# Kernel optimization log

Hardware: AMD Instinct MI355X
Metric: run time of the kernel (lower is better)

## Reference

```python
import jax, jax.numpy as jnp
import numpy as np

N_NODES = 50000
N_EDGES = 600000
F_IN = 128
F_HID = 128
F_OUT = 2


def setup_inputs() -> dict:
    key = jax.random.key(0)
    k_x, k_e, k_w1, k_w2 = jax.random.split(key, 4)
    x = jax.random.normal(k_x, (N_NODES, F_IN), dtype=jnp.float32)
    edge_index = jax.random.randint(k_e, (2, N_EDGES), 0, N_NODES, dtype=jnp.int32)
    # Glorot-style init for the GCNConv linear weights
    W1 = jax.random.normal(k_w1, (F_IN, F_HID), dtype=jnp.float32) * (1.0 / np.sqrt(F_IN))
    b1 = jnp.zeros((F_HID,), dtype=jnp.float32)
    W2 = jax.random.normal(k_w2, (F_HID, F_OUT), dtype=jnp.float32) * (1.0 / np.sqrt(F_HID))
    b2 = jnp.zeros((F_OUT,), dtype=jnp.float32)
    return {"x": x, "edge_index": edge_index, "W1": W1, "b1": b1, "W2": W2, "b2": b2}


def reference(x, edge_index, W1, b1, W2, b2):
    n = x.shape[0]
    # Add self-loops: A_tilde = A + I
    loops = jnp.arange(n, dtype=edge_index.dtype)
    src = jnp.concatenate([edge_index[0], loops])
    dst = jnp.concatenate([edge_index[1], loops])
    # Symmetric normalization: D^{-1/2} A_tilde D^{-1/2}
    deg = jax.ops.segment_sum(jnp.ones_like(dst, dtype=x.dtype), dst, num_segments=n)
    dinv = jnp.where(deg > 0, jax.lax.rsqrt(deg), 0.0)
    w = dinv[src] * dinv[dst]  # [E+N] per-edge norm coefficient

    def gcn_conv(h, W, b):
        h = h @ W  # transform first (small GEMM), then aggregate
        msg = h[src] * w[:, None]  # gather + scale, [E+N, F]
        return jax.ops.segment_sum(msg, dst, num_segments=n) + b

    h = jax.nn.relu(gcn_conv(x, W1, b1))
    # dropout is identity in eval mode
    return gcn_conv(h, W2, b2)
```

## Files before the change

kernel.cpp:

```cpp
#include <hip/hip_runtime.h>

#define N_NODES 50000
#define N_EDGES 600000
#define F 128
#define BCAP 64

typedef __attribute__((ext_vector_type(8))) short bf16x8;
typedef __attribute__((ext_vector_type(4))) float f32x4;

__device__ inline unsigned short bf16rn(float f) {
  unsigned u = __float_as_uint(f);
  return (unsigned short)((u + 0x7FFFu + ((u >> 16) & 1u)) >> 16);
}
__device__ inline float bflo(unsigned u) { return __uint_as_float(u << 16); }
__device__ inline float bfhi(unsigned u) { return __uint_as_float(u & 0xFFFF0000u); }

__global__ __launch_bounds__(256) void k_init(int* __restrict__ cnt, const float* __restrict__ W,
                                              ushort* __restrict__ wt, ushort* __restrict__ h,
                                              float* __restrict__ h2) {
  int i = blockIdx.x * 256 + threadIdx.x;
  if (i < N_NODES) cnt[i] = 0;
  if (i < F * F) {
    int n = i >> 7;
    int k = i & 127;
    wt[n * 128 + k] = bf16rn(W[k * 128 + n]);
  }
  if (i < F) h[(size_t)N_NODES * F + i] = 0;
  if (i == 0) { h2[2 * N_NODES] = 0.f; h2[2 * N_NODES + 1] = 0.f; }
}

__global__ __launch_bounds__(256) void k_fill(const int* __restrict__ ei, int* __restrict__ cnt,
                                              ushort* __restrict__ csr) {
  int e0 = (blockIdx.x * 256 + threadIdx.x) * 4;
  if (e0 >= N_EDGES) return;
  int4 s = *(const int4*)&ei[e0];
  int4 d = *(const int4*)&ei[N_EDGES + e0];
  int p0 = atomicAdd(&cnt[d.x], 1);
  int p1 = atomicAdd(&cnt[d.y], 1);
  int p2 = atomicAdd(&cnt[d.z], 1);
  int p3 = atomicAdd(&cnt[d.w], 1);
  if (p0 < BCAP) csr[d.x * BCAP + p0] = (ushort)s.x;
  if (p1 < BCAP) csr[d.y * BCAP + p1] = (ushort)s.y;
  if (p2 < BCAP) csr[d.z * BCAP + p2] = (ushort)s.z;
  if (p3 < BCAP) csr[d.w * BCAP + p3] = (ushort)s.w;
}

__global__ __launch_bounds__(256) void k_nodeinit(const int* __restrict__ cnt, float* __restrict__ dinv,
                                                  ushort* __restrict__ csr) {
  int i = blockIdx.x * 256 + threadIdx.x;
  if (i >= N_NODES) return;
  int c = min(cnt[i], BCAP);
  dinv[i] = rsqrtf((float)(c + 1));
  int npad = (c + 7) & ~7;
  for (int j = c; j < npad; ++j) csr[i * BCAP + j] = (ushort)N_NODES;
}

__global__ __launch_bounds__(256) void k_gemm1(const float* __restrict__ x, const ushort* __restrict__ wt_g,
                                               const float* __restrict__ dinv, ushort* __restrict__ h) {
  __shared__ ushort xs[64 * 128];
  __shared__ ushort wt[128 * 128];
  int t = threadIdx.x;
  int row0 = blockIdx.x * 64;

  {
    int r = t >> 2, q = t & 3;
    bool ok = (row0 + r) < N_NODES;
    const float4* xg = (const float4*)(x + (size_t)(row0 + r) * F + q * 32);
    unsigned pk[16];
    #pragma unroll
    for (int j = 0; j < 8; ++j) {
      float4 v = ok ? xg[j] : make_float4(0.f, 0.f, 0.f, 0.f);
      pk[2 * j]     = (unsigned)bf16rn(v.x) | ((unsigned)bf16rn(v.y) << 16);
      pk[2 * j + 1] = (unsigned)bf16rn(v.z) | ((unsigned)bf16rn(v.w) << 16);
    }
    #pragma unroll
    for (int j2 = 0; j2 < 4; ++j2) {
      int off = r * 256 + (((q * 64 + j2 * 16) ^ ((r & 7) << 4)));
      *(uint4*)((char*)xs + off) = make_uint4(pk[4 * j2], pk[4 * j2 + 1], pk[4 * j2 + 2], pk[4 * j2 + 3]);
    }
  }
  {
    int n = t >> 1, hf = t & 1;
    const uint4* wg = (const uint4*)(wt_g + n * 128);
    #pragma unroll
    for (int j = 0; j < 8; ++j) {
      uint4 v = wg[hf * 8 + j];
      int off = n * 256 + (((hf * 128 + j * 16) ^ ((n & 7) << 4)));
      *(uint4*)((char*)wt + off) = v;
    }
  }
  __syncthreads();

  int w = t >> 6;
  int lane = t & 63;
  int m = lane & 15;
  int kb = lane >> 4;
  int rloc = w * 16 + m;

  bf16x8 af[4];
  #pragma unroll
  for (int ks = 0; ks < 4; ++ks) {
    int off = rloc * 256 + (((ks * 64 + kb * 16) ^ ((rloc & 7) << 4)));
    af[ks] = *(bf16x8*)((char*)xs + off);
  }

  f32x4 acc[8];
  #pragma unroll
  for (int nf = 0; nf < 8; ++nf) acc[nf] = (f32x4){0.f, 0.f, 0.f, 0.f};

  #pragma unroll
  for (int nf = 0; nf < 8; ++nf) {
    int ncol = nf * 16 + m;
    #pragma unroll
    for (int ks = 0; ks < 4; ++ks) {
      int off = ncol * 256 + (((ks * 64 + kb * 16) ^ ((ncol & 7) << 4)));
      bf16x8 bfr = *(bf16x8*)((char*)wt + off);
      acc[nf] = __builtin_amdgcn_mfma_f32_16x16x32_bf16(af[ks], bfr, acc[nf], 0, 0, 0);
    }
  }

  int rbase = row0 + w * 16 + kb * 4;
  float di[4];
  #pragma unroll
  for (int reg = 0; reg < 4; ++reg) di[reg] = (rbase + reg < N_NODES) ? dinv[rbase + reg] : 0.f;
  #pragma unroll
  for (int nf = 0; nf < 8; ++nf) {
    #pragma unroll
    for (int reg = 0; reg < 4; ++reg) {
      int rr = rbase + reg;
      if (rr < N_NODES) h[(size_t)rr * F + nf * 16 + m] = bf16rn(di[reg] * acc[nf][reg]);
    }
  }
}

__global__ __launch_bounds__(256) void k_agg1(const uint4* __restrict__ h, const int* __restrict__ cnt,
                                              const float* __restrict__ dinv,
                                              const ushort* __restrict__ csr,
                                              const float* __restrict__ b1, const float* __restrict__ W2,
                                              float* __restrict__ h2) {
  int tid = threadIdx.x;
  int lane16 = tid & 15;
  int node = blockIdx.x * 16 + (tid >> 4);
  float di = dinv[node];
  uint4 su = h[(size_t)node * 16 + lane16];
  float a0 = bflo(su.x), a1 = bfhi(su.x), a2 = bflo(su.y), a3 = bfhi(su.y);
  float a4 = bflo(su.z), a5 = bfhi(su.z), a6 = bflo(su.w), a7 = bfhi(su.w);
  int base = node * BCAP;
  int npad = (min(cnt[node], BCAP) + 7) & ~7;
  for (int e = 0; e < npad; e += 8) {
    int s0 = csr[base + e + 0];
    int s1 = csr[base + e + 1];
    int s2 = csr[base + e + 2];
    int s3 = csr[base + e + 3];
    int s4 = csr[base + e + 4];
    int s5 = csr[base + e + 5];
    int s6 = csr[base + e + 6];
    int s7 = csr[base + e + 7];
    uint4 u0 = h[(size_t)s0 * 16 + lane16];
    uint4 u1 = h[(size_t)s1 * 16 + lane16];
    uint4 u2 = h[(size_t)s2 * 16 + lane16];
    uint4 u3 = h[(size_t)s3 * 16 + lane16];
    uint4 u4 = h[(size_t)s4 * 16 + lane16];
    uint4 u5 = h[(size_t)s5 * 16 + lane16];
    uint4 u6 = h[(size_t)s6 * 16 + lane16];
    uint4 u7 = h[(size_t)s7 * 16 + lane16];
    a0 += bflo(u0.x); a1 += bfhi(u0.x); a2 += bflo(u0.y); a3 += bfhi(u0.y);
    a4 += bflo(u0.z); a5 += bfhi(u0.z); a6 += bflo(u0.w); a7 += bfhi(u0.w);
    a0 += bflo(u1.x); a1 += bfhi(u1.x); a2 += bflo(u1.y); a3 += bfhi(u1.y);
    a4 += bflo(u1.z); a5 += bfhi(u1.z); a6 += bflo(u1.w); a7 += bfhi(u1.w);
    a0 += bflo(u2.x); a1 += bfhi(u2.x); a2 += bflo(u2.y); a3 += bfhi(u2.y);
    a4 += bflo(u2.z); a5 += bfhi(u2.z); a6 += bflo(u2.w); a7 += bfhi(u2.w);
    a0 += bflo(u3.x); a1 += bfhi(u3.x); a2 += bflo(u3.y); a3 += bfhi(u3.y);
    a4 += bflo(u3.z); a5 += bfhi(u3.z); a6 += bflo(u3.w); a7 += bfhi(u3.w);
    a0 += bflo(u4.x); a1 += bfhi(u4.x); a2 += bflo(u4.y); a3 += bfhi(u4.y);
    a4 += bflo(u4.z); a5 += bfhi(u4.z); a6 += bflo(u4.w); a7 += bfhi(u4.w);
    a0 += bflo(u5.x); a1 += bfhi(u5.x); a2 += bflo(u5.y); a3 += bfhi(u5.y);
    a4 += bflo(u5.z); a5 += bfhi(u5.z); a6 += bflo(u5.w); a7 += bfhi(u5.w);
    a0 += bflo(u6.x); a1 += bfhi(u6.x); a2 += bflo(u6.y); a3 += bfhi(u6.y);
    a4 += bflo(u6.z); a5 += bfhi(u6.z); a6 += bflo(u6.w); a7 += bfhi(u6.w);
    a0 += bflo(u7.x); a1 += bfhi(u7.x); a2 += bflo(u7.y); a3 += bfhi(u7.y);
    a4 += bflo(u7.z); a5 += bfhi(u7.z); a6 += bflo(u7.w); a7 += bfhi(u7.w);
  }
  float4 bb0 = ((const float4*)b1)[2 * lane16];
  float4 bb1 = ((const float4*)b1)[2 * lane16 + 1];
  float o0 = fmaxf(fmaf(di, a0, bb0.x), 0.f);
  float o1 = fmaxf(fmaf(di, a1, bb0.y), 0.f);
  float o2 = fmaxf(fmaf(di, a2, bb0.z), 0.f);
  float o3 = fmaxf(fmaf(di, a3, bb0.w), 0.f);
  float o4 = fmaxf(fmaf(di, a4, bb1.x), 0.f);
  float o5 = fmaxf(fmaf(di, a5, bb1.y), 0.f);
  float o6 = fmaxf(fmaf(di, a6, bb1.z), 0.f);
  float o7 = fmaxf(fmaf(di, a7, bb1.w), 0.f);

  const float2* W2v = (const float2*)W2;
  float2 w0 = W2v[8 * lane16 + 0], w1 = W2v[8 * lane16 + 1];
  float2 w2 = W2v[8 * lane16 + 2], w3 = W2v[8 * lane16 + 3];
  float2 w4 = W2v[8 * lane16 + 4], w5 = W2v[8 * lane16 + 5];
  float2 w6 = W2v[8 * lane16 + 6], w7 = W2v[8 * lane16 + 7];
  float c0 = fmaf(o0, w0.x, fmaf(o1, w1.x, fmaf(o2, w2.x, fmaf(o3, w3.x,
             fmaf(o4, w4.x, fmaf(o5, w5.x, fmaf(o6, w6.x, o7 * w7.x)))))));
  float c1 = fmaf(o0, w0.y, fmaf(o1, w1.y, fmaf(o2, w2.y, fmaf(o3, w3.y,
             fmaf(o4, w4.y, fmaf(o5, w5.y, fmaf(o6, w6.y, o7 * w7.y)))))));
  #pragma unroll
  for (int mask = 1; mask < 16; mask <<= 1) {
    c0 += __shfl_xor(c0, mask, 64);
    c1 += __shfl_xor(c1, mask, 64);
  }
  if (lane16 == 0) ((float2*)h2)[node] = make_float2(di * c0, di * c1);
}

__global__ __launch_bounds__(256) void k_agg2(const float* __restrict__ h2, const int* __restrict__ cnt,
                                              const float* __restrict__ dinv,
                                              const ushort* __restrict__ csr,
                                              const float* __restrict__ b2, float* __restrict__ out) {
  int i = blockIdx.x * 256 + threadIdx.x;
  if (i >= N_NODES) return;
  float di = dinv[i];
  const float2* hp = (const float2*)h2;
  float2 self = hp[i];
  float ax = self.x;
  float ay = self.y;
  int base = i * BCAP;
  int npad = (min(cnt[i], BCAP) + 3) & ~3;
  for (int e = 0; e < npad; e += 4) {
    int a = csr[base + e + 0];
    int b = csr[base + e + 1];
    int c = csr[base + e + 2];
    int d = csr[base + e + 3];
    float2 v0 = hp[a];
    float2 v1 = hp[b];
    float2 v2 = hp[c];
    float2 v3 = hp[d];
    ax += v0.x; ay += v0.y;
    ax += v1.x; ay += v1.y;
    ax += v2.x; ay += v2.y;
    ax += v3.x; ay += v3.y;
  }
  ((float2*)out)[i] = make_float2(fmaf(di, ax, b2[0]), fmaf(di, ay, b2[1]));
}

extern "C" void kernel_launch(void* const* d_in, const int* in_sizes, int n_in,
                              void* d_out, int out_size, void* d_ws, size_t ws_size,
                              hipStream_t stream) {
  const float* x  = (const float*)d_in[0];
  const int*   ei = (const int*)d_in[1];
  const float* W1 = (const float*)d_in[2];
  const float* b1 = (const float*)d_in[3];
  const float* W2 = (const float*)d_in[4];
  const float* b2 = (const float*)d_in[5];
  float* out = (float*)d_out;

  char* w = (char*)d_ws;
  auto alloc = [&](size_t bytes) {
    char* p = w;
    w += (bytes + 255) & ~size_t(255);
    return p;
  };
  int*    cnt  = (int*)alloc(N_NODES * 4);
  float*  dinv = (float*)alloc(N_NODES * 4);
  ushort* csr  = (ushort*)alloc((size_t)N_NODES * BCAP * 2);
  ushort* wt   = (ushort*)alloc((size_t)F * F * 2);
  ushort* h    = (ushort*)alloc((size_t)(N_NODES + 1) * F * 2);
  float*  h2   = (float*)alloc((size_t)(N_NODES + 1) * 2 * 4);

  k_init<<<196, 256, 0, stream>>>(cnt, W1, wt, h, h2);
  k_fill<<<586, 256, 0, stream>>>(ei, cnt, csr);
  k_nodeinit<<<196, 256, 0, stream>>>(cnt, dinv, csr);
  k_gemm1<<<782, 256, 0, stream>>>(x, wt, dinv, h);
  k_agg1<<<3125, 256, 0, stream>>>((const uint4*)h, cnt, dinv, csr, b1, W2, h2);
  k_agg2<<<196, 256, 0, stream>>>(h2, cnt, dinv, csr, b2, out);
}
```

Before: 95.30 us.

## Fuse node-init into GEMM1 and vectorize CSR index loads in aggregations

Folds the degree-normalization and CSR padding step into the GEMM kernel prologue, which removes one kernel launch and lets the per-row dinv come from shared memory. The aggregation kernels now read 8 (or 4) 16-bit neighbor indices with a single vector load instead of separate scalar loads. k_fill handles 8 edges per thread with half as many blocks. The gemm1 prologue adds a serial padding loop on 64 threads, and its dinv reads depend on an existing barrier in the GEMM body.

```diff
diff --git a/kernel.cpp b/kernel.cpp
--- a/kernel.cpp
+++ b/kernel.cpp
@@ -31,36 +31,50 @@
 
 __global__ __launch_bounds__(256) void k_fill(const int* __restrict__ ei, int* __restrict__ cnt,
                                               ushort* __restrict__ csr) {
-  int e0 = (blockIdx.x * 256 + threadIdx.x) * 4;
+  int e0 = (blockIdx.x * 256 + threadIdx.x) * 8;
   if (e0 >= N_EDGES) return;
-  int4 s = *(const int4*)&ei[e0];
-  int4 d = *(const int4*)&ei[N_EDGES + e0];
-  int p0 = atomicAdd(&cnt[d.x], 1);
-  int p1 = atomicAdd(&cnt[d.y], 1);
-  int p2 = atomicAdd(&cnt[d.z], 1);
-  int p3 = atomicAdd(&cnt[d.w], 1);
-  if (p0 < BCAP) csr[d.x * BCAP + p0] = (ushort)s.x;
-  if (p1 < BCAP) csr[d.y * BCAP + p1] = (ushort)s.y;
-  if (p2 < BCAP) csr[d.z * BCAP + p2] = (ushort)s.z;
-  if (p3 < BCAP) csr[d.w * BCAP + p3] = (ushort)s.w;
-}
-
-__global__ __launch_bounds__(256) void k_nodeinit(const int* __restrict__ cnt, float* __restrict__ dinv,
-                                                  ushort* __restrict__ csr) {
-  int i = blockIdx.x * 256 + threadIdx.x;
-  if (i >= N_NODES) return;
-  int c = min(cnt[i], BCAP);
-  dinv[i] = rsqrtf((float)(c + 1));
-  int npad = (c + 7) & ~7;
-  for (int j = c; j < npad; ++j) csr[i * BCAP + j] = (ushort)N_NODES;
+  int4 sa = *(const int4*)&ei[e0];
+  int4 sb = *(const int4*)&ei[e0 + 4];
+  int4 da = *(const int4*)&ei[N_EDGES + e0];
+  int4 db = *(const int4*)&ei[N_EDGES + e0 + 4];
+  int p0 = atomicAdd(&cnt[da.x], 1);
+  int p1 = atomicAdd(&cnt[da.y], 1);
+  int p2 = atomicAdd(&cnt[da.z], 1);
+  int p3 = atomicAdd(&cnt[da.w], 1);
+  int p4 = atomicAdd(&cnt[db.x], 1);
+  int p5 = atomicAdd(&cnt[db.y], 1);
+  int p6 = atomicAdd(&cnt[db.z], 1);
+  int p7 = atomicAdd(&cnt[db.w], 1);
+  if (p0 < BCAP) csr[da.x * BCAP + p0] = (ushort)sa.x;
+  if (p1 < BCAP) csr[da.y * BCAP + p1] = (ushort)sa.y;
+  if (p2 < BCAP) csr[da.z * BCAP + p2] = (ushort)sa.z;
+  if (p3 < BCAP) csr[da.w * BCAP + p3] = (ushort)sa.w;
+  if (p4 < BCAP) csr[db.x * BCAP + p4] = (ushort)sb.x;
+  if (p5 < BCAP) csr[db.y * BCAP + p5] = (ushort)sb.y;
+  if (p6 < BCAP) csr[db.z * BCAP + p6] = (ushort)sb.z;
+  if (p7 < BCAP) csr[db.w * BCAP + p7] = (ushort)sb.w;
 }
 
 __global__ __launch_bounds__(256) void k_gemm1(const float* __restrict__ x, const ushort* __restrict__ wt_g,
-                                               const float* __restrict__ dinv, ushort* __restrict__ h) {
+                                               const int* __restrict__ cnt, float* __restrict__ dinv,
+                                               ushort* __restrict__ csr, ushort* __restrict__ h) {
   __shared__ ushort xs[64 * 128];
   __shared__ ushort wt[128 * 128];
+  __shared__ float dinv_lds[64];
   int t = threadIdx.x;
   int row0 = blockIdx.x * 64;
+
+  if (t < 64) {
+    int node = row0 + t;
+    if (node < N_NODES) {
+      int c = min(cnt[node], BCAP);
+      float d = rsqrtf((float)(c + 1));
+      dinv_lds[t] = d;
+      dinv[node] = d;
+      int npad = (c + 7) & ~7;
+      for (int j = c; j < npad; ++j) csr[node * BCAP + j] = (ushort)N_NODES;
+    }
+  }
 
   {
     int r = t >> 2, q = t & 3;
@@ -120,15 +134,15 @@
   }
 
   int rbase = row0 + w * 16 + kb * 4;
-  float di[4];
-  #pragma unroll
-  for (int reg = 0; reg < 4; ++reg) di[reg] = (rbase + reg < N_NODES) ? dinv[rbase + reg] : 0.f;
   #pragma unroll
   for (int nf = 0; nf < 8; ++nf) {
     #pragma unroll
     for (int reg = 0; reg < 4; ++reg) {
       int rr = rbase + reg;
-      if (rr < N_NODES) h[(size_t)rr * F + nf * 16 + m] = bf16rn(di[reg] * acc[nf][reg]);
+      if (rr < N_NODES) {
+        float di = dinv_lds[w * 16 + kb * 4 + reg];
+        h[(size_t)rr * F + nf * 16 + m] = bf16rn(di * acc[nf][reg]);
+      }
     }
   }
 }
@@ -148,14 +162,11 @@
   int base = node * BCAP;
   int npad = (min(cnt[node], BCAP) + 7) & ~7;
   for (int e = 0; e < npad; e += 8) {
-    int s0 = csr[base + e + 0];
-    int s1 = csr[base + e + 1];
-    int s2 = csr[base + e + 2];
-    int s3 = csr[base + e + 3];
-    int s4 = csr[base + e + 4];
-    int s5 = csr[base + e + 5];
-    int s6 = csr[base + e + 6];
-    int s7 = csr[base + e + 7];
+    uint4 ci = *(const uint4*)&csr[base + e];
+    int s0 = ci.x & 0xFFFF, s1 = ci.x >> 16;
+    int s2 = ci.y & 0xFFFF, s3 = ci.y >> 16;
+    int s4 = ci.z & 0xFFFF, s5 = ci.z >> 16;
+    int s6 = ci.w & 0xFFFF, s7 = ci.w >> 16;
     uint4 u0 = h[(size_t)s0 * 16 + lane16];
     uint4 u1 = h[(size_t)s1 * 16 + lane16];
     uint4 u2 = h[(size_t)s2 * 16 + lane16];
@@ -223,10 +234,9 @@
   int base = i * BCAP;
   int npad = (min(cnt[i], BCAP) + 3) & ~3;
   for (int e = 0; e < npad; e += 4) {
-    int a = csr[base + e + 0];
-    int b = csr[base + e + 1];
-    int c = csr[base + e + 2];
-    int d = csr[base + e + 3];
+    uint2 ci = *(const uint2*)&csr[base + e];
+    int a = ci.x & 0xFFFF, b = ci.x >> 16;
+    int c = ci.y & 0xFFFF, d = ci.y >> 16;
     float2 v0 = hp[a];
     float2 v1 = hp[b];
     float2 v2 = hp[c];
@@ -264,9 +274,8 @@
   float*  h2   = (float*)alloc((size_t)(N_NODES + 1) * 2 * 4);
 
   k_init<<<196, 256, 0, stream>>>(cnt, W1, wt, h, h2);
-  k_fill<<<586, 256, 0, stream>>>(ei, cnt, csr);
-  k_nodeinit<<<196, 256, 0, stream>>>(cnt, dinv, csr);
-  k_gemm1<<<782, 256, 0, stream>>>(x, wt, dinv, h);
+  k_fill<<<293, 256, 0, stream>>>(ei, cnt, csr);
+  k_gemm1<<<782, 256, 0, stream>>>(x, wt, cnt, dinv, csr, h);
   k_agg1<<<3125, 256, 0, stream>>>((const uint4*)h, cnt, dinv, csr, b1, W2, h2);
   k_agg2<<<196, 256, 0, stream>>>(h2, cnt, dinv, csr, b2, out);
 }
```

After: 90.14 us, median of 2. -5.4%, faster.
